# Kernel tuning notes

Measured on AMD Instinct MI355X. Metric: run time of the kernel, lower is better.

Reference implementation:

```python
import jax, jax.numpy as jnp
import numpy as np


def _hadamard(n: int) -> np.ndarray:
    # Sylvester construction; n must be a power of 2 (asserted in the torch source).
    H = np.array([[1.0]], dtype=np.float32)
    while H.shape[0] < n:
        H = np.block([[H, H], [H, -H]])
    return (H * (n ** -0.5)).astype(np.float32)


def _rotate_activation(x):
    # hadamard_transform(x, scale=D**-0.5) over the last dim; bf16 in/out like the CUDA kernel.
    D = x.shape[-1]
    H = jnp.asarray(_hadamard(D))
    return (x.astype(jnp.float32) @ H).astype(x.dtype)


def _cu_seqlen_kv_bounds(seq_lens, num_ctx_tokens):
    # Vectorized equivalent of compute_cu_seqlen_kv_bounds_nocache (repeat_interleave -> searchsorted).
    offsets = jnp.concatenate([jnp.zeros(1, jnp.int32), jnp.cumsum(seq_lens).astype(jnp.int32)])
    pos = jnp.arange(num_ctx_tokens, dtype=jnp.int32)
    batch_ids = jnp.searchsorted(offsets, pos, side='right').astype(jnp.int32) - 1
    ks = offsets[batch_ids]                 # start of this token's sequence in packed KV
    ke = ks + (pos - ks) + 1                # causal: local_position + 1 past the start
    return ks, ke


def setup_inputs() -> dict:
    key = jax.random.key(0)
    k1, k2, k3 = jax.random.split(key, 3)
    T, H, D = 2048, 16, 128
    q = jax.random.normal(k1, (T, H, D), dtype=jnp.bfloat16)
    k = jax.random.normal(k2, (T, D), dtype=jnp.bfloat16)
    weights = jax.random.uniform(k3, (T, H), dtype=jnp.float32) * (H ** -0.5)
    seq_lens = jnp.array([1024, 1024], dtype=jnp.int32)
    return {"q": q, "k": k, "weights": weights, "seq_lens": seq_lens, "index_topk": 256}


def reference(q, k, weights, seq_lens, index_topk):
    T = q.shape[0]
    # Hadamard-rotate q and k (lightning indexer activation rotation).
    qr = _rotate_activation(q).astype(jnp.float32)   # [T, H, D]
    kr = _rotate_activation(k).astype(jnp.float32)   # [T, D]
    # Index score: I[t, s] = sum_h w[t, h] * relu(q[t, h] . k[s])
    logits = jnp.einsum('thd,sd->ths', qr, kr)       # [T, H, T]
    scores = jnp.einsum('ths,th->ts', jax.nn.relu(logits), weights)  # [T, T]
    # Causal ragged-batch KV window per token.
    ks, ke = _cu_seqlen_kv_bounds(seq_lens, T)
    pos = jnp.arange(T, dtype=jnp.int32)
    valid = (pos[None, :] >= ks[:, None]) & (pos[None, :] < ke[:, None])
    NEG = jnp.float32(-1e30)
    masked = jnp.where(valid, scores, NEG)
    topk_vals, topk_idx = jax.lax.top_k(masked, index_topk)  # [T, topk]
    return topk_vals, topk_idx
```

## Files before the change

### kernel.cpp

```cpp
#include <hip/hip_runtime.h>
#include <hip/hip_bf16.h>
#include <stdint.h>

typedef __attribute__((ext_vector_type(8))) short short8;
typedef __attribute__((ext_vector_type(4))) float float4_t;

#define DDIM 128
#define SORTN 256
#define LROW 136
#define SCAP 1088
#define NCHT 17

__device__ inline unsigned short f32_to_bf16_rne(float f) {
    uint32_t u = __float_as_uint(f);
    return (unsigned short)((u + 0x7FFFu + ((u >> 16) & 1u)) >> 16);
}
__device__ inline float bf16_to_f32(unsigned short h) {
    return __uint_as_float(((uint32_t)h) << 16);
}
__device__ inline int ks_of(const int* seq_lens, int n_seq, int t) {
    int off = 0, r = 0;
    for (int i = 0; i < n_seq; ++i) {
        int nx = off + seq_lens[i];
        if (t < nx) { r = off; break; }
        off = nx;
    }
    return r;
}

__device__ inline int wave_reduce_add_dpp(int x) {
    x += __builtin_amdgcn_update_dpp(0, x, 0x111, 0xF, 0xF, true);
    x += __builtin_amdgcn_update_dpp(0, x, 0x112, 0xF, 0xF, true);
    x += __builtin_amdgcn_update_dpp(0, x, 0x114, 0xF, 0xF, true);
    x += __builtin_amdgcn_update_dpp(0, x, 0x118, 0xF, 0xF, true);
    x += __builtin_amdgcn_update_dpp(0, x, 0x142, 0xA, 0xF, true);
    x += __builtin_amdgcn_update_dpp(0, x, 0x143, 0xC, 0xF, true);
    return __builtin_amdgcn_readlane(x, 63);
}

__global__ __launch_bounds__(256) void rotate_k_kernel(
        const unsigned short* __restrict__ k, unsigned short* __restrict__ kr, int T) {
    int row = blockIdx.x * 16 + (threadIdx.x >> 4);
    if (row >= T) return;
    int l16 = threadIdx.x & 15;
    short8 in = *(const short8*)(k + (size_t)row * DDIM + 8 * l16);
    float f[8];
    #pragma unroll
    for (int j = 0; j < 8; ++j) f[j] = bf16_to_f32((unsigned short)in[j]);
    #pragma unroll
    for (int b = 1; b <= 4; b <<= 1)
        #pragma unroll
        for (int j = 0; j < 8; ++j)
            if (!(j & b)) { float a = f[j], c = f[j | b]; f[j] = a + c; f[j | b] = a - c; }
    #pragma unroll
    for (int m = 1; m <= 8; m <<= 1) {
        bool hi = (l16 & m) != 0;
        #pragma unroll
        for (int j = 0; j < 8; ++j) {
            float o = __shfl_xor(f[j], m, 64);
            f[j] = hi ? (o - f[j]) : (f[j] + o);
        }
    }
    const float sc = 0.08838834764831845f;
    short8 out;
    #pragma unroll
    for (int j = 0; j < 8; ++j) out[j] = (short)f32_to_bf16_rne(f[j] * sc);
    *(short8*)(kr + (size_t)row * DDIM + 8 * l16) = out;
}

__global__ __launch_bounds__(512, 4) void fused_kernel(
        const unsigned short* __restrict__ q,
        const unsigned short* __restrict__ kr,
        const float* __restrict__ w,
        const int* __restrict__ seq_lens, int n_seq,
        float* __restrict__ out_vals, float* __restrict__ out_idx,
        int T, int H, int K, int Tt) {
    __shared__ __align__(16) unsigned short bL[2][64 * LROW];
    __shared__ __align__(16) float scw[4][SCAP];

    const int tid  = threadIdx.x;
    const int wv   = tid >> 6, lane = tid & 63;
    const int tok  = wv & 3, half = wv >> 2;
    const int col  = lane & 15, kgrp = lane >> 4;
    const int srow = tid >> 4, sseg = tid & 15;

    const int m     = blockIdx.x;
    const int ttile = (m & 1) ? (Tt - 1 - (m >> 1)) : (m >> 1);
    const int tt0   = ttile * 4;
    const int t_w   = tt0 + tok;
    const bool wvalid = (t_w < T);
    const int t_c  = wvalid ? t_w : T - 1;
    const int ks_w = ks_of(seq_lens, n_seq, t_c);
    const int ke_w = t_c + 1;
    const int n    = ke_w - ks_w;

    const int bks    = ks_of(seq_lens, n_seq, tt0);
    const int bke    = (tt0 + 4 < T) ? (tt0 + 4) : T;
    const int nchunk = (bke - bks + 63) >> 6;

    short8 pre[2];
    #pragma unroll
    for (int it = 0; it < 2; ++it) {
        int gs = bks + srow + 32 * it; if (gs > T - 1) gs = T - 1;
        pre[it] = *(const short8*)(kr + (size_t)gs * DDIM + sseg * 8);
    }

    float f[4][8];
    const unsigned short* qrow = q + ((size_t)t_c * H + col) * DDIM + kgrp * 8;
    #pragma unroll
    for (int kk = 0; kk < 4; ++kk) {
        short8 v = *(const short8*)(qrow + kk * 32);
        #pragma unroll
        for (int j = 0; j < 8; ++j) f[kk][j] = bf16_to_f32((unsigned short)v[j]);
    }
    #pragma unroll
    for (int b = 1; b <= 4; b <<= 1)
        #pragma unroll
        for (int kk = 0; kk < 4; ++kk)
            #pragma unroll
            for (int j = 0; j < 8; ++j)
                if (!(j & b)) { float a = f[kk][j], c = f[kk][j | b];
                                f[kk][j] = a + c; f[kk][j | b] = a - c; }
    #pragma unroll
    for (int kk = 0; kk < 4; ++kk)
        #pragma unroll
        for (int j = 0; j < 8; ++j) {
            float o = __shfl_xor(f[kk][j], 16, 64);
            f[kk][j] = (kgrp & 1) ? (o - f[kk][j]) : (f[kk][j] + o);
        }
    #pragma unroll
    for (int kk = 0; kk < 4; ++kk)
        #pragma unroll
        for (int j = 0; j < 8; ++j) {
            float o = __shfl_xor(f[kk][j], 32, 64);
            f[kk][j] = (kgrp & 2) ? (o - f[kk][j]) : (f[kk][j] + o);
        }
    #pragma unroll
    for (int j = 0; j < 8; ++j) {
        { float a = f[0][j], c = f[1][j]; f[0][j] = a + c; f[1][j] = a - c; }
        { float a = f[2][j], c = f[3][j]; f[2][j] = a + c; f[3][j] = a - c; }
        { float a = f[0][j], c = f[2][j]; f[0][j] = a + c; f[2][j] = a - c; }
        { float a = f[1][j], c = f[3][j]; f[1][j] = a + c; f[3][j] = a - c; }
    }
    short8 afrag[4];
    const float scl = 0.08838834764831845f;
    #pragma unroll
    for (int kk = 0; kk < 4; ++kk)
        #pragma unroll
        for (int j = 0; j < 8; ++j)
            afrag[kk][j] = (short)f32_to_bf16_rne(f[kk][j] * scl);

    float w4[4];
    #pragma unroll
    for (int r = 0; r < 4; ++r) w4[r] = w[(size_t)t_c * H + kgrp * 4 + r];

    #pragma unroll
    for (int it = 0; it < 2; ++it)
        *(short8*)&bL[0][(srow + 32 * it) * LROW + sseg * 8] = pre[it];
    __syncthreads();

    for (int c = 0; c < nchunk; ++c) {
        const int kv0 = bks + c * 64;
        if (c + 1 < nchunk) {
            int kvn = kv0 + 64;
            #pragma unroll
            for (int it = 0; it < 2; ++it) {
                int gs = kvn + srow + 32 * it; if (gs > T - 1) gs = T - 1;
                pre[it] = *(const short8*)(kr + (size_t)gs * DDIM + sseg * 8);
            }
        }
        const unsigned short* sb = bL[c & 1];
        #pragma unroll
        for (int nth = 0; nth < 2; ++nth) {
            const int nt = half * 2 + nth;
            float4_t acc = {0.f, 0.f, 0.f, 0.f};
            #pragma unroll
            for (int kk = 0; kk < 4; ++kk) {
                short8 bf = *(const short8*)&sb[(nt * 16 + col) * LROW + kgrp * 8 + kk * 32];
                acc = __builtin_amdgcn_mfma_f32_16x16x32_bf16(afrag[kk], bf, acc, 0, 0, 0);
            }
            float p = 0.f;
            #pragma unroll
            for (int r = 0; r < 4; ++r) {
                float v = acc[r];
                v = v > 0.f ? v : 0.f;
                p += w4[r] * v;
            }
            p += __shfl_xor(p, 16, 64);
            p += __shfl_xor(p, 32, 64);
            int s = kv0 + nt * 16 + col;
            if (wvalid && lane < 16 && s >= ks_w && s <= t_w)
                scw[tok][s - ks_w] = p;
        }
        if (c + 1 < nchunk) {
            #pragma unroll
            for (int it = 0; it < 2; ++it)
                *(short8*)&bL[(c + 1) & 1][(srow + 32 * it) * LROW + sseg * 8] = pre[it];
        }
        __syncthreads();
    }

    if (half == 1 || !wvalid) return;

    const int nch = (n + 63) >> 6;
    uint32_t ukey[NCHT];
    #pragma unroll
    for (int c = 0; c < NCHT; ++c) {
        if (c < nch) {
            int i = c * 64 + lane;
            ukey[c] = (i < n) ? __float_as_uint(scw[tok][i]) : 0u;
        } else ukey[c] = 0u;
    }
    unsigned long long* candw = (unsigned long long*)&scw[tok][0];

    const int Keff = (n < K) ? n : K;
    uint32_t ustar = 0;
    int ttake = K;
    if (n > K) {
        uint32_t lo = 0, hi = 0x80000000u;
        for (int it = 0; it < 31; ++it) {
            uint32_t mid = (lo + hi) >> 1;
            int lc = 0;
            #pragma unroll
            for (int c = 0; c < NCHT; ++c)
                if (c < nch) lc += (ukey[c] >= mid) ? 1 : 0;
            int total = wave_reduce_add_dpp(lc);
            if (total >= K) lo = mid; else hi = mid;
        }
        ustar = lo;
        int lg = 0;
        #pragma unroll
        for (int c = 0; c < NCHT; ++c)
            if (c < nch) lg += (ukey[c] > ustar) ? 1 : 0;
        ttake = K - wave_reduce_add_dpp(lg);
    }

    {
        const unsigned long long ltm = (1ull << lane) - 1ull;
        int base = 0, tieBase = 0;
        const bool selAll = (n <= K);
        #pragma unroll
        for (int c = 0; c < NCHT; ++c) {
            if (c < nch) {
                int i = c * 64 + lane;
                bool inb = (i < n);
                uint32_t u = ukey[c];
                bool isGt  = inb && (selAll || u > ustar);
                bool isTie = inb && !selAll && (u == ustar);
                unsigned long long mt = __ballot(isTie);
                int tr = tieBase + (int)__popcll(mt & ltm);
                bool take = isGt || (isTie && tr < ttake);
                unsigned long long mk = __ballot(take);
                if (take) {
                    int pos = base + (int)__popcll(mk & ltm);
                    int s = ks_w + i;
                    if (pos < SORTN)
                        candw[pos] = ((((unsigned long long)u << 11) |
                                       (unsigned long long)(T - 1 - s)) + 1ull);
                }
                base    += (int)__popcll(mk);
                tieBase += (int)__popcll(mt);
            }
        }
        for (int i = Keff + lane; i < SORTN; i += 64) candw[i] = 0ull;
    }

    unsigned long long kreg[4];
    #pragma unroll
    for (int r = 0; r < 4; ++r) kreg[r] = candw[4 * lane + r];

    #define CX(a, b, dsc) { unsigned long long _mx = (a) > (b) ? (a) : (b); \
                            unsigned long long _mn = (a) > (b) ? (b) : (a); \
                            (a) = (dsc) ? _mx : _mn; (b) = (dsc) ? _mn : _mx; }
    #pragma unroll
    for (int size = 2; size <= SORTN; size <<= 1) {
        #pragma unroll
        for (int stride = SORTN >> 1; stride >= 4; stride >>= 1) {
            if (stride > (size >> 1)) continue;
            int lmask = stride >> 2;
            #pragma unroll
            for (int r = 0; r < 4; ++r) {
                int e = 4 * lane + r;
                unsigned long long other = __shfl_xor(kreg[r], lmask, 64);
                bool desc = ((e & size) == 0);
                bool iAmLow = ((e & stride) == 0);
                bool keepMax = (iAmLow == desc);
                kreg[r] = keepMax ? (kreg[r] > other ? kreg[r] : other)
                                  : (kreg[r] < other ? kreg[r] : other);
            }
        }
        if (size >= 4) {
            bool d = (((4 * lane) & size) == 0);
            CX(kreg[0], kreg[2], d);
            CX(kreg[1], kreg[3], d);
            CX(kreg[0], kreg[1], d);
            CX(kreg[2], kreg[3], d);
        } else {
            CX(kreg[0], kreg[1], true);
            CX(kreg[2], kreg[3], false);
        }
    }
    #undef CX

    if (4 * lane < K) {
        float4_t v4, i4;
        #pragma unroll
        for (int r = 0; r < 4; ++r) {
            int e = 4 * lane + r;
            unsigned long long key = kreg[r];
            float v; int idx;
            if (key != 0ull) {
                unsigned long long km1 = key - 1ull;
                v = __uint_as_float((uint32_t)(km1 >> 11));
                idx = T - 1 - (int)(km1 & 0x7FFull);
            } else {
                int pidx = e - Keff;
                idx = (pidx < ks_w) ? pidx : (ke_w + (pidx - ks_w));
                v = -1e30f;
            }
            v4[r] = v; i4[r] = (float)idx;
        }
        *(float4_t*)(out_vals + (size_t)t_w * K + 4 * lane) = v4;
        *(float4_t*)(out_idx  + (size_t)t_w * K + 4 * lane) = i4;
    }
}

extern "C" void kernel_launch(void* const* d_in, const int* in_sizes, int n_in,
                              void* d_out, int out_size, void* d_ws, size_t ws_size,
                              hipStream_t stream) {
    const unsigned short* q = (const unsigned short*)d_in[0];
    const unsigned short* k = (const unsigned short*)d_in[1];
    const float* w          = (const float*)d_in[2];
    const int* seq_lens     = (const int*)d_in[3];
    const int n_seq = in_sizes[3];
    const int T = in_sizes[1] / DDIM;
    const int H = in_sizes[2] / T;
    const int K = out_size / (2 * T);

    unsigned short* kr = (unsigned short*)d_ws;
    float* out_vals = (float*)d_out;
    float* out_idx  = out_vals + (size_t)T * K;

    rotate_k_kernel<<<dim3((T + 15) / 16), dim3(256), 0, stream>>>(k, kr, T);
    const int Tt = (T + 3) / 4;
    fused_kernel<<<dim3(Tt), dim3(512), 0, stream>>>(
        q, kr, w, seq_lens, n_seq, out_vals, out_idx, T, H, K, Tt);
}
```

Before: 104.6 us.

## Give each wave its own token and stream K straight from global memory

The block-cooperative design is replaced. Previously 8 waves shared double-buffered LDS tiles of rotated K for 4 adjacent tokens. Now each wave independently handles one token, strided across blocks, and loads its K fragments directly from global memory. Scores are staged per 64-column chunk through a small shared scratch buffer into registers, which removes block-wide syncs and the large LDS footprint. The key-register array is sized by a template split (16 vs 32 chunks), which also raises the supported sequence length. The cost is no LDS reuse of K across tokens, more global/L2 traffic per wave, and uncoalesced fragment loads.

```diff
diff --git a/kernel.cpp b/kernel.cpp
--- a/kernel.cpp
+++ b/kernel.cpp
@@ -7,9 +7,6 @@
 
 #define DDIM 128
 #define SORTN 256
-#define LROW 136
-#define SCAP 1088
-#define NCHT 17
 
 __device__ inline unsigned short f32_to_bf16_rne(float f) {
     uint32_t u = __float_as_uint(f);
@@ -68,45 +65,18 @@
     *(short8*)(kr + (size_t)row * DDIM + 8 * l16) = out;
 }
 
-__global__ __launch_bounds__(512, 4) void fused_kernel(
+template <int NCHT>
+__device__ __forceinline__ void wave_token_work(
+        int t, int ks, int n, int T, int H, int K,
         const unsigned short* __restrict__ q,
         const unsigned short* __restrict__ kr,
         const float* __restrict__ w,
-        const int* __restrict__ seq_lens, int n_seq,
+        volatile float* scratch64,
+        unsigned long long* candw,
         float* __restrict__ out_vals, float* __restrict__ out_idx,
-        int T, int H, int K, int Tt) {
-    __shared__ __align__(16) unsigned short bL[2][64 * LROW];
-    __shared__ __align__(16) float scw[4][SCAP];
-
-    const int tid  = threadIdx.x;
-    const int wv   = tid >> 6, lane = tid & 63;
-    const int tok  = wv & 3, half = wv >> 2;
-    const int col  = lane & 15, kgrp = lane >> 4;
-    const int srow = tid >> 4, sseg = tid & 15;
-
-    const int m     = blockIdx.x;
-    const int ttile = (m & 1) ? (Tt - 1 - (m >> 1)) : (m >> 1);
-    const int tt0   = ttile * 4;
-    const int t_w   = tt0 + tok;
-    const bool wvalid = (t_w < T);
-    const int t_c  = wvalid ? t_w : T - 1;
-    const int ks_w = ks_of(seq_lens, n_seq, t_c);
-    const int ke_w = t_c + 1;
-    const int n    = ke_w - ks_w;
-
-    const int bks    = ks_of(seq_lens, n_seq, tt0);
-    const int bke    = (tt0 + 4 < T) ? (tt0 + 4) : T;
-    const int nchunk = (bke - bks + 63) >> 6;
-
-    short8 pre[2];
-    #pragma unroll
-    for (int it = 0; it < 2; ++it) {
-        int gs = bks + srow + 32 * it; if (gs > T - 1) gs = T - 1;
-        pre[it] = *(const short8*)(kr + (size_t)gs * DDIM + sseg * 8);
-    }
-
+        int lane, int col, int kgrp) {
     float f[4][8];
-    const unsigned short* qrow = q + ((size_t)t_c * H + col) * DDIM + kgrp * 8;
+    const unsigned short* qrow = q + ((size_t)t * H + col) * DDIM + kgrp * 8;
     #pragma unroll
     for (int kk = 0; kk < 4; ++kk) {
         short8 v = *(const short8*)(qrow + kk * 32);
@@ -152,66 +122,39 @@
 
     float w4[4];
     #pragma unroll
-    for (int r = 0; r < 4; ++r) w4[r] = w[(size_t)t_c * H + kgrp * 4 + r];
-
-    #pragma unroll
-    for (int it = 0; it < 2; ++it)
-        *(short8*)&bL[0][(srow + 32 * it) * LROW + sseg * 8] = pre[it];
-    __syncthreads();
-
-    for (int c = 0; c < nchunk; ++c) {
-        const int kv0 = bks + c * 64;
-        if (c + 1 < nchunk) {
-            int kvn = kv0 + 64;
+    for (int r = 0; r < 4; ++r) w4[r] = w[(size_t)t * H + kgrp * 4 + r];
+
+    const int nchunk = (n + 63) >> 6;
+    uint32_t ukey[NCHT];
+    #pragma unroll
+    for (int c = 0; c < NCHT; ++c) {
+        if (c < nchunk) {
+            const int s0 = ks + c * 64;
             #pragma unroll
-            for (int it = 0; it < 2; ++it) {
-                int gs = kvn + srow + 32 * it; if (gs > T - 1) gs = T - 1;
-                pre[it] = *(const short8*)(kr + (size_t)gs * DDIM + sseg * 8);
+            for (int j = 0; j < 4; ++j) {
+                int sa = s0 + 16 * j + col;
+                if (sa > T - 1) sa = T - 1;
+                const short8* kb = (const short8*)(kr + (size_t)sa * DDIM + kgrp * 8);
+                float4_t acc = {0.f, 0.f, 0.f, 0.f};
+                acc = __builtin_amdgcn_mfma_f32_16x16x32_bf16(afrag[0], kb[0],  acc, 0, 0, 0);
+                acc = __builtin_amdgcn_mfma_f32_16x16x32_bf16(afrag[1], kb[4],  acc, 0, 0, 0);
+                acc = __builtin_amdgcn_mfma_f32_16x16x32_bf16(afrag[2], kb[8],  acc, 0, 0, 0);
+                acc = __builtin_amdgcn_mfma_f32_16x16x32_bf16(afrag[3], kb[12], acc, 0, 0, 0);
+                float p = 0.f;
+                #pragma unroll
+                for (int r = 0; r < 4; ++r) {
+                    float v = acc[r];
+                    v = v > 0.f ? v : 0.f;
+                    p += w4[r] * v;
+                }
+                p += __shfl_xor(p, 16, 64);
+                p += __shfl_xor(p, 32, 64);
+                if (lane < 16) scratch64[16 * j + lane] = p;
             }
-        }
-        const unsigned short* sb = bL[c & 1];
-        #pragma unroll
-        for (int nth = 0; nth < 2; ++nth) {
-            const int nt = half * 2 + nth;
-            float4_t acc = {0.f, 0.f, 0.f, 0.f};
-            #pragma unroll
-            for (int kk = 0; kk < 4; ++kk) {
-                short8 bf = *(const short8*)&sb[(nt * 16 + col) * LROW + kgrp * 8 + kk * 32];
-                acc = __builtin_amdgcn_mfma_f32_16x16x32_bf16(afrag[kk], bf, acc, 0, 0, 0);
-            }
-            float p = 0.f;
-            #pragma unroll
-            for (int r = 0; r < 4; ++r) {
-                float v = acc[r];
-                v = v > 0.f ? v : 0.f;
-                p += w4[r] * v;
-            }
-            p += __shfl_xor(p, 16, 64);
-            p += __shfl_xor(p, 32, 64);
-            int s = kv0 + nt * 16 + col;
-            if (wvalid && lane < 16 && s >= ks_w && s <= t_w)
-                scw[tok][s - ks_w] = p;
-        }
-        if (c + 1 < nchunk) {
-            #pragma unroll
-            for (int it = 0; it < 2; ++it)
-                *(short8*)&bL[(c + 1) & 1][(srow + 32 * it) * LROW + sseg * 8] = pre[it];
-        }
-        __syncthreads();
-    }
-
-    if (half == 1 || !wvalid) return;
-
-    const int nch = (n + 63) >> 6;
-    uint32_t ukey[NCHT];
-    #pragma unroll
-    for (int c = 0; c < NCHT; ++c) {
-        if (c < nch) {
-            int i = c * 64 + lane;
-            ukey[c] = (i < n) ? __float_as_uint(scw[tok][i]) : 0u;
+            float sv = scratch64[lane];
+            ukey[c] = (c * 64 + lane < n) ? __float_as_uint(sv) : 0u;
         } else ukey[c] = 0u;
     }
-    unsigned long long* candw = (unsigned long long*)&scw[tok][0];
 
     const int Keff = (n < K) ? n : K;
     uint32_t ustar = 0;
@@ -223,7 +166,7 @@
             int lc = 0;
             #pragma unroll
             for (int c = 0; c < NCHT; ++c)
-                if (c < nch) lc += (ukey[c] >= mid) ? 1 : 0;
+                if (c < nchunk) lc += (ukey[c] >= mid) ? 1 : 0;
             int total = wave_reduce_add_dpp(lc);
             if (total >= K) lo = mid; else hi = mid;
         }
@@ -231,7 +174,7 @@
         int lg = 0;
         #pragma unroll
         for (int c = 0; c < NCHT; ++c)
-            if (c < nch) lg += (ukey[c] > ustar) ? 1 : 0;
+            if (c < nchunk) lg += (ukey[c] > ustar) ? 1 : 0;
         ttake = K - wave_reduce_add_dpp(lg);
     }
 
@@ -241,7 +184,7 @@
         const bool selAll = (n <= K);
         #pragma unroll
         for (int c = 0; c < NCHT; ++c) {
-            if (c < nch) {
+            if (c < nchunk) {
                 int i = c * 64 + lane;
                 bool inb = (i < n);
                 uint32_t u = ukey[c];
@@ -253,7 +196,7 @@
                 unsigned long long mk = __ballot(take);
                 if (take) {
                     int pos = base + (int)__popcll(mk & ltm);
-                    int s = ks_w + i;
+                    int s = ks + i;
                     if (pos < SORTN)
                         candw[pos] = ((((unsigned long long)u << 11) |
                                        (unsigned long long)(T - 1 - s)) + 1ull);
@@ -315,14 +258,39 @@
                 idx = T - 1 - (int)(km1 & 0x7FFull);
             } else {
                 int pidx = e - Keff;
-                idx = (pidx < ks_w) ? pidx : (ke_w + (pidx - ks_w));
+                idx = (pidx < ks) ? pidx : ((t + 1) + (pidx - ks));
                 v = -1e30f;
             }
             v4[r] = v; i4[r] = (float)idx;
         }
-        *(float4_t*)(out_vals + (size_t)t_w * K + 4 * lane) = v4;
-        *(float4_t*)(out_idx  + (size_t)t_w * K + 4 * lane) = i4;
-    }
+        *(float4_t*)(out_vals + (size_t)t * K + 4 * lane) = v4;
+        *(float4_t*)(out_idx  + (size_t)t * K + 4 * lane) = i4;
+    }
+}
+
+__global__ __launch_bounds__(256, 2) void fused2_kernel(
+        const unsigned short* __restrict__ q,
+        const unsigned short* __restrict__ kr,
+        const float* __restrict__ w,
+        const int* __restrict__ seq_lens, int n_seq,
+        float* __restrict__ out_vals, float* __restrict__ out_idx,
+        int T, int H, int K, int NB) {
+    __shared__ float scratch[4][64];
+    __shared__ unsigned long long cand[4][SORTN];
+
+    const int wv = threadIdx.x >> 6, lane = threadIdx.x & 63;
+    const int col = lane & 15, kgrp = lane >> 4;
+    const int t = (int)blockIdx.x + NB * wv;
+    if (t >= T) return;
+    const int ks = ks_of(seq_lens, n_seq, t);
+    const int n  = t + 1 - ks;
+
+    if (n <= 64 * 16)
+        wave_token_work<16>(t, ks, n, T, H, K, q, kr, w,
+                            scratch[wv], cand[wv], out_vals, out_idx, lane, col, kgrp);
+    else
+        wave_token_work<32>(t, ks, n, T, H, K, q, kr, w,
+                            scratch[wv], cand[wv], out_vals, out_idx, lane, col, kgrp);
 }
 
 extern "C" void kernel_launch(void* const* d_in, const int* in_sizes, int n_in,
@@ -342,7 +310,7 @@
     float* out_idx  = out_vals + (size_t)T * K;
 
     rotate_k_kernel<<<dim3((T + 15) / 16), dim3(256), 0, stream>>>(k, kr, T);
-    const int Tt = (T + 3) / 4;
-    fused_kernel<<<dim3(Tt), dim3(512), 0, stream>>>(
-        q, kr, w, seq_lens, n_seq, out_vals, out_idx, T, H, K, Tt);
-}
+    const int NB = (T + 3) / 4;
+    fused2_kernel<<<dim3(NB), dim3(256), 0, stream>>>(
+        q, kr, w, seq_lens, n_seq, out_vals, out_idx, T, H, K, NB);
+}
```

Result: slower. 128.5 us (+22.9%).
